# Kernel tuning notes

Measured on AMD Instinct MI355X. Metric: run time of the kernel, lower is better.

## Reference

```python
import jax, jax.numpy as jnp
import numpy as np

DIM = 1536
NUM_HEADS = 24
HEAD_DIM = DIM // NUM_HEADS
SCALE = HEAD_DIM ** -0.5
B, NX, NC = 2, 2048, 256


def setup_inputs() -> dict:
    key = jax.random.key(0)
    ks = jax.random.split(key, 12)
    s = 0.02
    return {
        "x": jax.random.normal(ks[0], (B, NX, DIM), jnp.float32),
        "c": jax.random.normal(ks[1], (B, NC, DIM), jnp.float32),
        "Wqkv_x": jax.random.normal(ks[2], (3 * DIM, DIM), jnp.float32) * s,
        "bqkv_x": jax.random.normal(ks[3], (3 * DIM,), jnp.float32) * s,
        "Wqkv_c": jax.random.normal(ks[4], (3 * DIM, DIM), jnp.float32) * s,
        "bqkv_c": jax.random.normal(ks[5], (3 * DIM,), jnp.float32) * s,
        "Wproj_x": jax.random.normal(ks[6], (DIM, DIM), jnp.float32) * s,
        "bproj_x": jax.random.normal(ks[7], (DIM,), jnp.float32) * s,
        "Wproj_c": jax.random.normal(ks[8], (DIM, DIM), jnp.float32) * s,
        "bproj_c": jax.random.normal(ks[9], (DIM,), jnp.float32) * s,
    }


def _qkv(t, W, b):
    # t: [B, N, C] -> q, k, v each [B, H, N, Dh]
    Bt, N, C = t.shape
    qkv = (t @ W.T + b).reshape(Bt, N, 3, NUM_HEADS, HEAD_DIM)
    qkv = jnp.transpose(qkv, (2, 0, 3, 1, 4))  # [3, B, H, N, Dh]
    return qkv[0], qkv[1], qkv[2]


def reference(x, c, Wqkv_x, bqkv_x, Wqkv_c, bqkv_c, Wproj_x, bproj_x, Wproj_c, bproj_c):
    q_x, k_x, v_x = _qkv(x, Wqkv_x, bqkv_x)
    q_c, k_c, v_c = _qkv(c, Wqkv_c, bqkv_c)
    q = jnp.concatenate([q_x, q_c], axis=2)  # [B, H, Nx+Nc, Dh]
    k = jnp.concatenate([k_x, k_c], axis=2)
    v = jnp.concatenate([v_x, v_c], axis=2)
    attn = jnp.einsum("bhnd,bhmd->bhnm", q, k) * SCALE
    attn = jax.nn.softmax(attn, axis=-1)
    out = jnp.einsum("bhnm,bhmd->bhnd", attn, v)  # [B, H, N, Dh]
    x_out = out[:, :, :NX]
    c_out = out[:, :, NX:]
    x_out = jnp.transpose(x_out, (0, 2, 1, 3)).reshape(x.shape[0], NX, DIM)
    c_out = jnp.transpose(c_out, (0, 2, 1, 3)).reshape(c.shape[0], NC, DIM)
    return (x_out @ Wproj_x.T + bproj_x, c_out @ Wproj_c.T + bproj_c)
```

## Files before the change

### kernel.cpp

```cpp
#include <hip/hip_runtime.h>
#include <stdint.h>

#define HNUM 24
#define DIMX 1536
#define NXT  2048
#define NCT  256
#define NTOT 2304
#define BB   2

typedef __attribute__((ext_vector_type(8))) short bf16x8;
typedef __attribute__((ext_vector_type(8))) _Float16 f16x8;
typedef __attribute__((ext_vector_type(4))) _Float16 f16x4;
typedef __attribute__((ext_vector_type(2))) _Float16 f16x2;
typedef __attribute__((ext_vector_type(2))) __fp16 hp16x2;
typedef __attribute__((ext_vector_type(4))) float f32x4;
typedef __attribute__((ext_vector_type(4))) unsigned short u16x4;

#define AS1 __attribute__((address_space(1)))
#define AS3 __attribute__((address_space(3)))

__device__ __forceinline__ void glds16(const void* g, void* l) {
  __builtin_amdgcn_global_load_lds((AS1 void*)(uintptr_t)g, (AS3 void*)l, 16, 0, 0);
}

__device__ __forceinline__ unsigned short f2bf(float f) {
  unsigned int u = __float_as_uint(f);
  u += 0x7FFFu + ((u >> 16) & 1u);
  return (unsigned short)(u >> 16);
}

__device__ __forceinline__ f16x2 pkrtz(float a, float b) {
  hp16x2 r = __builtin_amdgcn_cvt_pkrtz(a, b);
  union { hp16x2 h; f16x2 f; } u;
  u.h = r;
  return u.f;
}

__device__ __forceinline__ bf16x8 ldfragB(const unsigned short* S, int row, int cc) {
  return *(const bf16x8*)(S + row * 64 + ((cc ^ (row & 7)) << 3));
}
__device__ __forceinline__ f16x8 ldVfrag8(const _Float16* S, int row, int mbp, int quad) {
  int cc = (quad * 2 + mbp) ^ (row & 7);
  return *(const f16x8*)(S + row * 64 + cc * 8);
}

struct CastDesc { const float* src; unsigned short* dst; int start4; };
struct CastArgs { CastDesc d[6]; int total4; };

__global__ __launch_bounds__(256) void cast_all(CastArgs a) {
  int i = blockIdx.x * 256 + threadIdx.x;
  if (i >= a.total4) return;
  int r = 0;
#pragma unroll
  for (int k = 1; k < 6; ++k) r += (i >= a.d[k].start4);
  int j = i - a.d[r].start4;
  float4 v = reinterpret_cast<const float4*>(a.d[r].src)[j];
  u16x4 o;
  o[0] = f2bf(v.x); o[1] = f2bf(v.y); o[2] = f2bf(v.z); o[3] = f2bf(v.w);
  reinterpret_cast<u16x4*>(a.d[r].dst)[j] = o;
}

__device__ __forceinline__ void gemm_mainloop(
    const unsigned short* __restrict__ Ablk,
    const unsigned short* __restrict__ Wblk,
    unsigned short* As, unsigned short* Bs, f32x4 acc[4][4]) {
  const int tid  = threadIdx.x;
  const int lane = tid & 63;
  const int quad = lane >> 4, l16 = lane & 15;
  const int wave = tid >> 6;
  const int wm = (wave >> 1) * 64, wo = (wave & 1) * 64;

  for (int k0 = 0; k0 < DIMX; k0 += 64) {
    __syncthreads();
#pragma unroll
    for (int p = 0; p < 4; ++p) {
      int c = p * 256 + tid;
      int row = c >> 3;
      int kc = ((c & 7) ^ (row & 7)) << 3;
      glds16(Ablk + (size_t)row * DIMX + k0 + kc, As + c * 8);
      glds16(Wblk + (size_t)row * DIMX + k0 + kc, Bs + c * 8);
    }
    __syncthreads();
#pragma unroll
    for (int kk = 0; kk < 64; kk += 32) {
      bf16x8 af[4], bf[4];
#pragma unroll
      for (int mb = 0; mb < 4; ++mb)
        af[mb] = ldfragB(As, wm + mb * 16 + l16, (kk >> 3) + quad);
#pragma unroll
      for (int ob = 0; ob < 4; ++ob)
        bf[ob] = ldfragB(Bs, wo + ob * 16 + l16, (kk >> 3) + quad);
#pragma unroll
      for (int mb = 0; mb < 4; ++mb)
#pragma unroll
        for (int ob = 0; ob < 4; ++ob)
          acc[mb][ob] = __builtin_amdgcn_mfma_f32_16x16x32_bf16(
              af[mb], bf[ob], acc[mb][ob], 0, 0, 0);
    }
  }
}

__global__ __launch_bounds__(256, 3) void gemm_qkv(
    const unsigned short* __restrict__ xbf, const unsigned short* __restrict__ cbf,
    const unsigned short* __restrict__ Wx, const unsigned short* __restrict__ Wc,
    const float* __restrict__ bx_, const float* __restrict__ bc_,
    unsigned short* __restrict__ Qb, unsigned short* __restrict__ Kb,
    _Float16* __restrict__ VTf) {
  __shared__ unsigned short Sh[2][128 * 64];
  unsigned short* As = Sh[0];
  unsigned short* Bs = Sh[1];

  const bool isC = blockIdx.y >= 32;
  const int yloc = isC ? (int)blockIdx.y - 32 : (int)blockIdx.y;
  const int tokShift = isC ? 8 : 11;
  const int seqOff = isC ? NXT : 0;
  const unsigned short* A = (isC ? cbf : xbf) + (size_t)yloc * 128 * DIMX;
  const unsigned short* W = (isC ? Wc : Wx) + (size_t)blockIdx.x * 128 * DIMX;
  const float* bias = isC ? bc_ : bx_;

  const f32x4 z4 = {0.f, 0.f, 0.f, 0.f};
  f32x4 acc[4][4];
#pragma unroll
  for (int i = 0; i < 4; ++i)
#pragma unroll
    for (int j = 0; j < 4; ++j) acc[i][j] = z4;

  gemm_mainloop(A, W, As, Bs, acc);

  const int tid = threadIdx.x, lane = tid & 63, wave = tid >> 6;
  const int quad = lane >> 4, l16 = lane & 15;
  const int wm = (wave >> 1) * 64, wo = (wave & 1) * 64;
  const int s = blockIdx.x / 12;
  const float QSC = 0.125f * 1.44269504088896340736f;

  float bv[4];
#pragma unroll
  for (int ob = 0; ob < 4; ++ob)
    bv[ob] = bias[blockIdx.x * 128 + wo + ob * 16 + l16];

  if (s < 2) {
#pragma unroll
    for (int ob = 0; ob < 4; ++ob) {
      int o = blockIdx.x * 128 + wo + ob * 16 + l16;
      int rem = o - s * DIMX;
      int h = rem >> 6, d = rem & 63;
#pragma unroll
      for (int mb = 0; mb < 4; ++mb) {
#pragma unroll
        for (int r = 0; r < 4; ++r) {
          int m = yloc * 128 + wm + mb * 16 + quad * 4 + r;
          int b = m >> tokShift;
          int n = seqOff + (m & ((1 << tokShift) - 1));
          size_t bh = (size_t)b * HNUM + h;
          float v = acc[mb][ob][r] + bv[ob];
          if (s == 0) Qb[(bh * NTOT + n) * 64 + d] = f2bf(v * QSC);
          else        Kb[(bh * NTOT + n) * 64 + d] = f2bf(v);
        }
      }
    }
  } else {
    _Float16* Ts = (_Float16*)Sh;
    __syncthreads();
#pragma unroll
    for (int ob = 0; ob < 4; ++ob) {
      int dloc = wo + ob * 16 + l16;
      int sw = (dloc & 15) << 3;
#pragma unroll
      for (int mb = 0; mb < 4; ++mb) {
        f16x4 pk;
#pragma unroll
        for (int r = 0; r < 4; ++r) pk[r] = (_Float16)(acc[mb][ob][r] + bv[ob]);
        int m0 = wm + mb * 16 + quad * 4;
        *(f16x4*)(Ts + dloc * 128 + (m0 ^ sw)) = pk;
      }
    }
    __syncthreads();
#pragma unroll
    for (int it = 0; it < 8; ++it) {
      int cth = it * 256 + tid;
      int d = cth >> 4;
      int m0 = (cth & 15) << 3;
      f16x8 val = *(const f16x8*)(Ts + d * 128 + (m0 ^ ((d & 15) << 3)));
      int dglob = (blockIdx.x - 24) * 128 + d;
      int h = dglob >> 6, dd = dglob & 63;
      int M = yloc * 128 + m0;
      int b = M >> tokShift;
      int n = seqOff + (M & ((1 << tokShift) - 1));
      *(f16x8*)(VTf + ((size_t)(b * HNUM + h) * 64 + dd) * NTOT + n) = val;
    }
  }
}

__global__ __launch_bounds__(256, 3) void gemm_proj(
    const unsigned short* __restrict__ AX, const unsigned short* __restrict__ AC,
    const unsigned short* __restrict__ Wx, const unsigned short* __restrict__ Wc,
    const float* __restrict__ bx_, const float* __restrict__ bc_,
    float* __restrict__ out) {
  __shared__ unsigned short As[128 * 64];
  __shared__ unsigned short Bs[128 * 64];

  const bool isC = blockIdx.y >= 32;
  const int yloc = isC ? (int)blockIdx.y - 32 : (int)blockIdx.y;
  const unsigned short* A = (isC ? AC : AX) + (size_t)yloc * 128 * DIMX;
  const unsigned short* W = (isC ? Wc : Wx) + (size_t)blockIdx.x * 128 * DIMX;
  const float* bias = isC ? bc_ : bx_;
  float* o_ = out + (isC ? (size_t)BB * NXT * DIMX : (size_t)0) +
              (size_t)yloc * 128 * DIMX;

  const f32x4 z4 = {0.f, 0.f, 0.f, 0.f};
  f32x4 acc[4][4];
#pragma unroll
  for (int i = 0; i < 4; ++i)
#pragma unroll
    for (int j = 0; j < 4; ++j) acc[i][j] = z4;

  gemm_mainloop(A, W, As, Bs, acc);

  const int lane = threadIdx.x & 63, wave = threadIdx.x >> 6;
  const int quad = lane >> 4, l16 = lane & 15;
  const int wm = (wave >> 1) * 64, wo = (wave & 1) * 64;

#pragma unroll
  for (int ob = 0; ob < 4; ++ob) {
    int o = blockIdx.x * 128 + wo + ob * 16 + l16;
    float bv = bias[o];
#pragma unroll
    for (int mb = 0; mb < 4; ++mb) {
#pragma unroll
      for (int r = 0; r < 4; ++r) {
        int m = wm + mb * 16 + quad * 4 + r;
        o_[(size_t)m * DIMX + o] = acc[mb][ob][r] + bv;
      }
    }
  }
}

__global__ __launch_bounds__(512, 4) void flash_attn(
    const unsigned short* __restrict__ Qb, const unsigned short* __restrict__ Kb,
    const _Float16* __restrict__ Vf,
    unsigned short* __restrict__ AX, unsigned short* __restrict__ AC) {
  __shared__ unsigned short Ks[2][64 * 64];
  __shared__ _Float16      Vs[2][64 * 64];

  const int tid = threadIdx.x, lane = tid & 63, wave = tid >> 6;
  const int quad = lane >> 4, l16 = lane & 15;
  const int bh = blockIdx.y;
  const int qbase = blockIdx.x * 256 + wave * 32;

  bf16x8 qf[2][2];
#pragma unroll
  for (int qb = 0; qb < 2; ++qb)
#pragma unroll
    for (int kh = 0; kh < 2; ++kh)
      qf[qb][kh] = *(const bf16x8*)(
          Qb + ((size_t)bh * NTOT + qbase + qb * 16 + l16) * 64 + kh * 32 + quad * 8);

  const f32x4 z4 = {0.f, 0.f, 0.f, 0.f};
  f32x4 accT[2][4];
  f32x4 lacc[2];
#pragma unroll
  for (int qb = 0; qb < 2; ++qb) {
    lacc[qb] = z4;
#pragma unroll
    for (int db = 0; db < 4; ++db) accT[qb][db] = z4;
  }

  const size_t kbase = (size_t)bh * NTOT * 64;
  const size_t vbase = (size_t)bh * 64 * NTOT;
  const f16x4 ones4 = {(_Float16)1.f, (_Float16)1.f, (_Float16)1.f, (_Float16)1.f};

  const int srow = tid >> 3, scc = tid & 7;
  const int squad = scc >> 1, smbp = scc & 1;
  const int skv = 32 * smbp + squad * 4;
  _Float16* const sdst0 = &Vs[0][0] + srow * 64 + ((scc ^ (srow & 7)) << 3);
  _Float16* const sdst1 = &Vs[1][0] + srow * 64 + ((scc ^ (srow & 7)) << 3);
  const _Float16* const vsrc = Vf + vbase + (size_t)srow * NTOT + skv;

  f16x4 vstg0, vstg1;
  auto loadV = [&](int kt) {
    vstg0 = *(const f16x4*)(vsrc + kt * 64);
    vstg1 = *(const f16x4*)(vsrc + kt * 64 + 16);
  };
  auto writeV = [&](int kt) {
    f16x8 w;
    w[0] = vstg0[0]; w[1] = vstg0[1]; w[2] = vstg0[2]; w[3] = vstg0[3];
    w[4] = vstg1[0]; w[5] = vstg1[1]; w[6] = vstg1[2]; w[7] = vstg1[3];
    *(f16x8*)((kt & 1) ? sdst1 : sdst0) = w;
  };
  auto stageK = [&](int kt) {
    const int kv0 = kt * 64;
    int row = tid >> 3;
    int kc = ((tid & 7) ^ (row & 7)) << 3;
    glds16(Kb + kbase + (size_t)(kv0 + row) * 64 + kc, &Ks[kt & 1][0] + tid * 8);
  };

  loadV(0);
  stageK(0);
  writeV(0);
  for (int kt = 0; kt < 36; ++kt) {
    __syncthreads();
    if (kt < 35) { loadV(kt + 1); stageK(kt + 1); }
    const unsigned short* K_ = &Ks[kt & 1][0];
    const _Float16*       V_ = &Vs[kt & 1][0];

    f32x4 st[2][4];
#pragma unroll
    for (int qb = 0; qb < 2; ++qb)
#pragma unroll
      for (int mb = 0; mb < 4; ++mb) st[qb][mb] = z4;
    __builtin_amdgcn_s_setprio(1);
#pragma unroll
    for (int kh = 0; kh < 2; ++kh) {
#pragma unroll
      for (int mb = 0; mb < 4; ++mb) {
        bf16x8 kf = ldfragB(K_, mb * 16 + l16, kh * 4 + quad);
#pragma unroll
        for (int qb = 0; qb < 2; ++qb)
          st[qb][mb] = __builtin_amdgcn_mfma_f32_16x16x32_bf16(
              kf, qf[qb][kh], st[qb][mb], 0, 0, 0);
      }
    }
    __builtin_amdgcn_s_setprio(0);

    f16x4 pf[2][4];
#pragma unroll
    for (int qb = 0; qb < 2; ++qb) {
#pragma unroll
      for (int mb = 0; mb < 4; ++mb) {
        float p0 = __builtin_amdgcn_exp2f(st[qb][mb][0]);
        float p1 = __builtin_amdgcn_exp2f(st[qb][mb][1]);
        float p2 = __builtin_amdgcn_exp2f(st[qb][mb][2]);
        float p3 = __builtin_amdgcn_exp2f(st[qb][mb][3]);
        f16x2 lo = pkrtz(p0, p1);
        f16x2 hi = pkrtz(p2, p3);
        f16x4 pk = {lo[0], lo[1], hi[0], hi[1]};
        pf[qb][mb] = pk;
        lacc[qb] = __builtin_amdgcn_mfma_f32_16x16x16f16(
            ones4, pk, lacc[qb], 0, 0, 0);
      }
    }

    if (kt < 35) writeV(kt + 1);

    __builtin_amdgcn_s_setprio(1);
#pragma unroll
    for (int db = 0; db < 4; ++db) {
#pragma unroll
      for (int mbp = 0; mbp < 2; ++mbp) {
        f16x8 v2 = ldVfrag8(V_, db * 16 + l16, mbp, quad);
        f16x4 vlo = {v2[0], v2[1], v2[2], v2[3]};
        f16x4 vhi = {v2[4], v2[5], v2[6], v2[7]};
#pragma unroll
        for (int qb = 0; qb < 2; ++qb)
          accT[qb][db] = __builtin_amdgcn_mfma_f32_16x16x16f16(
              vlo, pf[qb][2 * mbp], accT[qb][db], 0, 0, 0);
#pragma unroll
        for (int qb = 0; qb < 2; ++qb)
          accT[qb][db] = __builtin_amdgcn_mfma_f32_16x16x16f16(
              vhi, pf[qb][2 * mbp + 1], accT[qb][db], 0, 0, 0);
      }
    }
    __builtin_amdgcn_s_setprio(0);
  }

  float inv[2];
#pragma unroll
  for (int qb = 0; qb < 2; ++qb) inv[qb] = __frcp_rn(lacc[qb][0]);

  const int b = bh / HNUM, h = bh - b * HNUM;
#pragma unroll
  for (int qb = 0; qb < 2; ++qb) {
    int n = qbase + qb * 16 + l16;
#pragma unroll
    for (int db = 0; db < 4; ++db) {
      u16x4 o;
#pragma unroll
      for (int r = 0; r < 4; ++r) o[r] = f2bf(accT[qb][db][r] * inv[qb]);
      int col = h * 64 + db * 16 + quad * 4;
      if (n < NXT)
        *(u16x4*)(AX + ((size_t)b * NXT + n) * DIMX + col) = o;
      else
        *(u16x4*)(AC + ((size_t)b * NCT + (n - NXT)) * DIMX + col) = o;
    }
  }
}

extern "C" void kernel_launch(void* const* d_in, const int* in_sizes, int n_in,
                              void* d_out, int out_size, void* d_ws, size_t ws_size,
                              hipStream_t stream) {
  const float* x       = (const float*)d_in[0];
  const float* c       = (const float*)d_in[1];
  const float* Wqkv_x  = (const float*)d_in[2];
  const float* bqkv_x  = (const float*)d_in[3];
  const float* Wqkv_c  = (const float*)d_in[4];
  const float* bqkv_c  = (const float*)d_in[5];
  const float* Wproj_x = (const float*)d_in[6];
  const float* bproj_x = (const float*)d_in[7];
  const float* Wproj_c = (const float*)d_in[8];
  const float* bproj_c = (const float*)d_in[9];
  float* out = (float*)d_out;

  char* ws = (char*)d_ws;
  size_t off = 0;
  auto alloc = [&](size_t nelem) {
    unsigned short* p = (unsigned short*)(ws + off);
    off += nelem * 2;
    return p;
  };
  unsigned short* xbf  = alloc((size_t)BB * NXT * DIMX);
  unsigned short* cbf  = alloc((size_t)BB * NCT * DIMX);
  unsigned short* wqx  = alloc((size_t)3 * DIMX * DIMX);
  unsigned short* wqc  = alloc((size_t)3 * DIMX * DIMX);
  unsigned short* wpx  = alloc((size_t)DIMX * DIMX);
  unsigned short* wpc  = alloc((size_t)DIMX * DIMX);
  unsigned short* Qb   = alloc((size_t)BB * HNUM * NTOT * 64);
  unsigned short* Kb   = alloc((size_t)BB * HNUM * NTOT * 64);
  _Float16*       VTf  = (_Float16*)alloc((size_t)BB * HNUM * NTOT * 64);
  unsigned short* AX   = alloc((size_t)BB * NXT * DIMX);
  unsigned short* AC   = alloc((size_t)BB * NCT * DIMX);

  CastArgs ca;
  const float* srcs[6] = {x, c, Wqkv_x, Wqkv_c, Wproj_x, Wproj_c};
  unsigned short* dsts[6] = {xbf, cbf, wqx, wqc, wpx, wpc};
  size_t ns[6] = {(size_t)BB * NXT * DIMX, (size_t)BB * NCT * DIMX,
                  (size_t)3 * DIMX * DIMX, (size_t)3 * DIMX * DIMX,
                  (size_t)DIMX * DIMX, (size_t)DIMX * DIMX};
  int acc4 = 0;
  for (int i = 0; i < 6; ++i) {
    ca.d[i].src = srcs[i];
    ca.d[i].dst = dsts[i];
    ca.d[i].start4 = acc4;
    acc4 += (int)(ns[i] / 4);
  }
  ca.total4 = acc4;
  cast_all<<<dim3((acc4 + 255) / 256), dim3(256), 0, stream>>>(ca);

  gemm_qkv<<<dim3(36, 36), dim3(256), 0, stream>>>(xbf, cbf, wqx, wqc,
                                                   bqkv_x, bqkv_c, Qb, Kb, VTf);

  flash_attn<<<dim3(9, 48), dim3(512), 0, stream>>>(Qb, Kb, VTf, AX, AC);

  gemm_proj<<<dim3(12, 36), dim3(256), 0, stream>>>(AX, AC, wpx, wpc,
                                                    bproj_x, bproj_c, out);
}
```

Baseline: 340.7 us.

## Use 256x128 GEMM tiles with triple-buffered async LDS pipeline and XCD swizzle

Both GEMMs move from 128x128 tiles with 256 threads and a synchronous single-buffer loop to 256x128 tiles with 512 threads. The new loop keeps three LDS stages, issues loads two k-steps ahead interleaved with MFMA, and raises wave priority during MFMA. Blocks are launched on a 1-D grid whose index is remapped so neighbouring tiles land on the same XCD for L2 reuse. The aim is to hide global-load latency and cut barrier stalls. The cost is 144KB of LDS per block and fewer resident blocks. The V-transpose epilogue is resized to the larger tile.

Result: no change. 339.9 us (-0.2%).

```diff
diff --git a/kernel.cpp b/kernel.cpp
--- a/kernel.cpp
+++ b/kernel.cpp
@@ -7,6 +7,7 @@
 #define NCT  256
 #define NTOT 2304
 #define BB   2
+#define NK   (DIMX / 64)
 
 typedef __attribute__((ext_vector_type(8))) short bf16x8;
 typedef __attribute__((ext_vector_type(8))) _Float16 f16x8;
@@ -60,7 +61,7 @@
   reinterpret_cast<u16x4*>(a.d[r].dst)[j] = o;
 }
 
-__device__ __forceinline__ void gemm_mainloop(
+__device__ __forceinline__ void gemm_mainloop256(
     const unsigned short* __restrict__ Ablk,
     const unsigned short* __restrict__ Wblk,
     unsigned short* As, unsigned short* Bs, f32x4 acc[4][4]) {
@@ -70,52 +71,80 @@
   const int wave = tid >> 6;
   const int wm = (wave >> 1) * 64, wo = (wave & 1) * 64;
 
-  for (int k0 = 0; k0 < DIMX; k0 += 64) {
-    __syncthreads();
-#pragma unroll
-    for (int p = 0; p < 4; ++p) {
-      int c = p * 256 + tid;
-      int row = c >> 3;
-      int kc = ((c & 7) ^ (row & 7)) << 3;
-      glds16(Ablk + (size_t)row * DIMX + k0 + kc, As + c * 8);
-      glds16(Wblk + (size_t)row * DIMX + k0 + kc, Bs + c * 8);
-    }
-    __syncthreads();
-#pragma unroll
-    for (int kk = 0; kk < 64; kk += 32) {
-      bf16x8 af[4], bf[4];
+  auto stageA = [&](int kt, int buf, int i) {
+    int c = i * 512 + tid;
+    int row = c >> 3;
+    int kc = ((c & 7) ^ (row & 7)) << 3;
+    glds16(Ablk + (size_t)row * DIMX + kt * 64 + kc, As + buf * (256 * 64) + c * 8);
+  };
+  auto stageB = [&](int kt, int buf, int i) {
+    int c = i * 512 + tid;
+    int row = c >> 3;
+    int kc = ((c & 7) ^ (row & 7)) << 3;
+    glds16(Wblk + (size_t)row * DIMX + kt * 64 + kc, Bs + buf * (128 * 64) + c * 8);
+  };
+
+  stageA(0, 0, 0); stageA(0, 0, 1); stageA(0, 0, 2); stageA(0, 0, 3);
+  stageB(0, 0, 0); stageB(0, 0, 1);
+  stageA(1, 1, 0); stageA(1, 1, 1); stageA(1, 1, 2); stageA(1, 1, 3);
+  stageB(1, 1, 0); stageB(1, 1, 1);
+  asm volatile("s_waitcnt vmcnt(6)" ::: "memory");
+  __builtin_amdgcn_s_barrier();
+
+  int cur = 0;
+  for (int kt = 0; kt < NK; ++kt) {
+    const unsigned short* A_ = As + cur * (256 * 64);
+    const unsigned short* B_ = Bs + cur * (128 * 64);
+    const int stg = (cur == 0) ? 2 : cur - 1;
+    const bool doStage = (kt + 2 < NK);
+#pragma unroll
+    for (int kk = 0; kk < 2; ++kk) {
+      bf16x8 af[4], bfr[4];
 #pragma unroll
       for (int mb = 0; mb < 4; ++mb)
-        af[mb] = ldfragB(As, wm + mb * 16 + l16, (kk >> 3) + quad);
+        af[mb] = ldfragB(A_, wm + mb * 16 + l16, kk * 4 + quad);
 #pragma unroll
       for (int ob = 0; ob < 4; ++ob)
-        bf[ob] = ldfragB(Bs, wo + ob * 16 + l16, (kk >> 3) + quad);
+        bfr[ob] = ldfragB(B_, wo + ob * 16 + l16, kk * 4 + quad);
+      if (doStage) {
+        if (kk == 0) { stageA(kt + 2, stg, 0); stageA(kt + 2, stg, 1); stageA(kt + 2, stg, 2); }
+        else         { stageA(kt + 2, stg, 3); stageB(kt + 2, stg, 0); stageB(kt + 2, stg, 1); }
+      }
+      __builtin_amdgcn_s_setprio(1);
 #pragma unroll
       for (int mb = 0; mb < 4; ++mb)
 #pragma unroll
         for (int ob = 0; ob < 4; ++ob)
           acc[mb][ob] = __builtin_amdgcn_mfma_f32_16x16x32_bf16(
-              af[mb], bf[ob], acc[mb][ob], 0, 0, 0);
-    }
-  }
-}
-
-__global__ __launch_bounds__(256, 3) void gemm_qkv(
+              af[mb], bfr[ob], acc[mb][ob], 0, 0, 0);
+      __builtin_amdgcn_s_setprio(0);
+    }
+    if (doStage)          asm volatile("s_waitcnt vmcnt(6)" ::: "memory");
+    else if (kt + 1 < NK) asm volatile("s_waitcnt vmcnt(0)" ::: "memory");
+    __builtin_amdgcn_s_barrier();
+    cur = (cur == 2) ? 0 : cur + 1;
+  }
+}
+
+__global__ __launch_bounds__(512, 2) void gemm_qkv(
     const unsigned short* __restrict__ xbf, const unsigned short* __restrict__ cbf,
     const unsigned short* __restrict__ Wx, const unsigned short* __restrict__ Wc,
     const float* __restrict__ bx_, const float* __restrict__ bc_,
     unsigned short* __restrict__ Qb, unsigned short* __restrict__ Kb,
     _Float16* __restrict__ VTf) {
-  __shared__ unsigned short Sh[2][128 * 64];
-  unsigned short* As = Sh[0];
-  unsigned short* Bs = Sh[1];
-
-  const bool isC = blockIdx.y >= 32;
-  const int yloc = isC ? (int)blockIdx.y - 32 : (int)blockIdx.y;
+  __shared__ unsigned short SA[3][256 * 64];
+  __shared__ unsigned short SB[3][128 * 64];
+
+  const int swz = ((int)blockIdx.x & 7) * (648 / 8) + ((int)blockIdx.x >> 3);
+  const int bx = swz % 36;
+  const int by = swz / 36;
+
+  const bool isC = by >= 16;
+  const int yloc = isC ? by - 16 : by;
   const int tokShift = isC ? 8 : 11;
   const int seqOff = isC ? NXT : 0;
-  const unsigned short* A = (isC ? cbf : xbf) + (size_t)yloc * 128 * DIMX;
-  const unsigned short* W = (isC ? Wc : Wx) + (size_t)blockIdx.x * 128 * DIMX;
+  const unsigned short* A = (isC ? cbf : xbf) + (size_t)yloc * 256 * DIMX;
+  const unsigned short* W = (isC ? Wc : Wx) + (size_t)bx * 128 * DIMX;
   const float* bias = isC ? bc_ : bx_;
 
   const f32x4 z4 = {0.f, 0.f, 0.f, 0.f};
@@ -125,30 +154,30 @@
 #pragma unroll
     for (int j = 0; j < 4; ++j) acc[i][j] = z4;
 
-  gemm_mainloop(A, W, As, Bs, acc);
+  gemm_mainloop256(A, W, &SA[0][0], &SB[0][0], acc);
 
   const int tid = threadIdx.x, lane = tid & 63, wave = tid >> 6;
   const int quad = lane >> 4, l16 = lane & 15;
   const int wm = (wave >> 1) * 64, wo = (wave & 1) * 64;
-  const int s = blockIdx.x / 12;
+  const int s = bx / 12;
   const float QSC = 0.125f * 1.44269504088896340736f;
 
   float bv[4];
 #pragma unroll
   for (int ob = 0; ob < 4; ++ob)
-    bv[ob] = bias[blockIdx.x * 128 + wo + ob * 16 + l16];
+    bv[ob] = bias[bx * 128 + wo + ob * 16 + l16];
 
   if (s < 2) {
 #pragma unroll
     for (int ob = 0; ob < 4; ++ob) {
-      int o = blockIdx.x * 128 + wo + ob * 16 + l16;
+      int o = bx * 128 + wo + ob * 16 + l16;
       int rem = o - s * DIMX;
       int h = rem >> 6, d = rem & 63;
 #pragma unroll
       for (int mb = 0; mb < 4; ++mb) {
 #pragma unroll
         for (int r = 0; r < 4; ++r) {
-          int m = yloc * 128 + wm + mb * 16 + quad * 4 + r;
+          int m = yloc * 256 + wm + mb * 16 + quad * 4 + r;
           int b = m >> tokShift;
           int n = seqOff + (m & ((1 << tokShift) - 1));
           size_t bh = (size_t)b * HNUM + h;
@@ -159,31 +188,31 @@
       }
     }
   } else {
-    _Float16* Ts = (_Float16*)Sh;
+    _Float16* Ts = (_Float16*)SA;
     __syncthreads();
 #pragma unroll
     for (int ob = 0; ob < 4; ++ob) {
       int dloc = wo + ob * 16 + l16;
-      int sw = (dloc & 15) << 3;
+      int sw = (dloc & 31) << 3;
 #pragma unroll
       for (int mb = 0; mb < 4; ++mb) {
         f16x4 pk;
 #pragma unroll
         for (int r = 0; r < 4; ++r) pk[r] = (_Float16)(acc[mb][ob][r] + bv[ob]);
         int m0 = wm + mb * 16 + quad * 4;
-        *(f16x4*)(Ts + dloc * 128 + (m0 ^ sw)) = pk;
+        *(f16x4*)(Ts + dloc * 256 + (m0 ^ sw)) = pk;
       }
     }
     __syncthreads();
 #pragma unroll
     for (int it = 0; it < 8; ++it) {
-      int cth = it * 256 + tid;
-      int d = cth >> 4;
-      int m0 = (cth & 15) << 3;
-      f16x8 val = *(const f16x8*)(Ts + d * 128 + (m0 ^ ((d & 15) << 3)));
-      int dglob = (blockIdx.x - 24) * 128 + d;
+      int cth = it * 512 + tid;
+      int d = cth >> 5;
+      int m0 = (cth & 31) << 3;
+      f16x8 val = *(const f16x8*)(Ts + d * 256 + (m0 ^ ((d & 31) << 3)));
+      int dglob = (bx - 24) * 128 + d;
       int h = dglob >> 6, dd = dglob & 63;
-      int M = yloc * 128 + m0;
+      int M = yloc * 256 + m0;
       int b = M >> tokShift;
       int n = seqOff + (M & ((1 << tokShift) - 1));
       *(f16x8*)(VTf + ((size_t)(b * HNUM + h) * 64 + dd) * NTOT + n) = val;
@@ -191,21 +220,25 @@
   }
 }
 
-__global__ __launch_bounds__(256, 3) void gemm_proj(
+__global__ __launch_bounds__(512, 2) void gemm_proj(
     const unsigned short* __restrict__ AX, const unsigned short* __restrict__ AC,
     const unsigned short* __restrict__ Wx, const unsigned short* __restrict__ Wc,
     const float* __restrict__ bx_, const float* __restrict__ bc_,
     float* __restrict__ out) {
-  __shared__ unsigned short As[128 * 64];
-  __shared__ unsigned short Bs[128 * 64];
-
-  const bool isC = blockIdx.y >= 32;
-  const int yloc = isC ? (int)blockIdx.y - 32 : (int)blockIdx.y;
-  const unsigned short* A = (isC ? AC : AX) + (size_t)yloc * 128 * DIMX;
-  const unsigned short* W = (isC ? Wc : Wx) + (size_t)blockIdx.x * 128 * DIMX;
+  __shared__ unsigned short SA[3][256 * 64];
+  __shared__ unsigned short SB[3][128 * 64];
+
+  const int swz = ((int)blockIdx.x & 7) * (216 / 8) + ((int)blockIdx.x >> 3);
+  const int bx = swz % 12;
+  const int by = swz / 12;
+
+  const bool isC = by >= 16;
+  const int yloc = isC ? by - 16 : by;
+  const unsigned short* A = (isC ? AC : AX) + (size_t)yloc * 256 * DIMX;
+  const unsigned short* W = (isC ? Wc : Wx) + (size_t)bx * 128 * DIMX;
   const float* bias = isC ? bc_ : bx_;
   float* o_ = out + (isC ? (size_t)BB * NXT * DIMX : (size_t)0) +
-              (size_t)yloc * 128 * DIMX;
+              (size_t)yloc * 256 * DIMX;
 
   const f32x4 z4 = {0.f, 0.f, 0.f, 0.f};
   f32x4 acc[4][4];
@@ -214,7 +247,7 @@
 #pragma unroll
     for (int j = 0; j < 4; ++j) acc[i][j] = z4;
 
-  gemm_mainloop(A, W, As, Bs, acc);
+  gemm_mainloop256(A, W, &SA[0][0], &SB[0][0], acc);
 
   const int lane = threadIdx.x & 63, wave = threadIdx.x >> 6;
   const int quad = lane >> 4, l16 = lane & 15;
@@ -222,7 +255,7 @@
 
 #pragma unroll
   for (int ob = 0; ob < 4; ++ob) {
-    int o = blockIdx.x * 128 + wo + ob * 16 + l16;
+    int o = bx * 128 + wo + ob * 16 + l16;
     float bv = bias[o];
 #pragma unroll
     for (int mb = 0; mb < 4; ++mb) {
@@ -435,11 +468,11 @@
   ca.total4 = acc4;
   cast_all<<<dim3((acc4 + 255) / 256), dim3(256), 0, stream>>>(ca);
 
-  gemm_qkv<<<dim3(36, 36), dim3(256), 0, stream>>>(xbf, cbf, wqx, wqc,
-                                                   bqkv_x, bqkv_c, Qb, Kb, VTf);
+  gemm_qkv<<<dim3(648), dim3(512), 0, stream>>>(xbf, cbf, wqx, wqc,
+                                                bqkv_x, bqkv_c, Qb, Kb, VTf);
 
   flash_attn<<<dim3(9, 48), dim3(512), 0, stream>>>(Qb, Kb, VTf, AX, AC);
 
-  gemm_proj<<<dim3(12, 36), dim3(256), 0, stream>>>(AX, AC, wpx, wpc,
-                                                    bproj_x, bproj_c, out);
-}
+  gemm_proj<<<dim3(216), dim3(512), 0, stream>>>(AX, AC, wpx, wpc,
+                                                 bproj_x, bproj_c, out);
+}
```
